# Kernel tuning notes

Hardware: AMD Instinct MI355X
Metric: run time of the kernel (lower is better)

The kernel has to match this reference:

```python
import jax, jax.numpy as jnp
import numpy as np

C = 256
RED = 8
DQK = C // RED  # 32


def setup_inputs() -> dict:
    key = jax.random.key(0)
    ks = jax.random.split(key, 8)
    B, H, W = 8, 64, 64
    x = jax.random.normal(ks[0], (B, C, H, W), dtype=jnp.float32)
    # 1x1 conv weights stored as [out, in]; biases [out]
    Wq = jax.random.normal(ks[1], (DQK, C), dtype=jnp.float32) * 0.02
    bq = jax.random.normal(ks[2], (DQK,), dtype=jnp.float32) * 0.02
    Wk = jax.random.normal(ks[3], (DQK, C), dtype=jnp.float32) * 0.02
    bk = jax.random.normal(ks[4], (DQK,), dtype=jnp.float32) * 0.02
    Wv = jax.random.normal(ks[5], (C, C), dtype=jnp.float32) * 0.02
    bv = jax.random.normal(ks[6], (C,), dtype=jnp.float32) * 0.02
    gamma = jax.random.normal(ks[7], (1,), dtype=jnp.float32) * 0.1
    return {"x": x, "Wq": Wq, "bq": bq, "Wk": Wk, "bk": bk, "Wv": Wv, "bv": bv, "gamma": gamma}


def reference(x, Wq, bq, Wk, bk, Wv, bv, gamma):
    B, Cc, H, W = x.shape
    N = H * W
    xf = x.reshape(B, Cc, N)                       # (B, C, N)
    # 1x1 convs == per-pixel dense projections
    q = jnp.einsum('dc,bcn->bdn', Wq, xf) + bq[None, :, None]   # (B, d, N)
    k = jnp.einsum('dc,bcn->bdn', Wk, xf) + bk[None, :, None]   # (B, d, N)
    v = jnp.einsum('ec,bcn->ben', Wv, xf) + bv[None, :, None]   # (B, C, N)
    # energy[b,i,j] = q[b,:,i] . k[b,:,j]; softmax over j (no scaling, SAGAN-style)
    energy = jnp.einsum('bdi,bdj->bij', q, k)      # (B, N, N)
    attn = jax.nn.softmax(energy, axis=-1)
    # out[b,c,i] = sum_j v[b,c,j] * attn[b,i,j]
    out = jnp.einsum('bcj,bij->bci', v, attn)      # (B, C, N)
    out = out.reshape(B, Cc, H, W)
    return gamma[0] * out + x
```

## Files before the change

kernel.cpp:

```cpp
#include <hip/hip_runtime.h>

#define NB 8
#define CCH 256
#define DQK 32
#define NPIX 4096

typedef __attribute__((ext_vector_type(8))) short short8;
typedef __attribute__((ext_vector_type(4))) float f32x4;

static __device__ __forceinline__ unsigned short f2bf(float f) {
  unsigned int u = __builtin_bit_cast(unsigned int, f);
  u += 0x7FFFu + ((u >> 16) & 1u);
  return (unsigned short)(u >> 16);
}

__global__ __launch_bounds__(256) void proj_kernel(
    const float* __restrict__ x,
    const float* __restrict__ Wq, const float* __restrict__ bq,
    const float* __restrict__ Wk, const float* __restrict__ bk,
    const float* __restrict__ Wv, const float* __restrict__ bv,
    unsigned short* __restrict__ Qb, unsigned short* __restrict__ Kb,
    unsigned short* __restrict__ Vb) {
  __shared__ unsigned short xs[CCH * 65];
  const int t = threadIdx.x;
  const int b = blockIdx.x >> 6;
  const int i0 = (blockIdx.x & 63) * 64;
  const float* xb = x + (size_t)b * CCH * NPIX + i0;
  {
    const int ii = (t & 15) * 4;
    const int cb = t >> 4;
#pragma unroll
    for (int rep = 0; rep < 16; ++rep) {
      const int c = cb + 16 * rep;
      const float4 v = *(const float4*)(xb + (size_t)c * NPIX + ii);
      unsigned short* dst = &xs[c * 65 + ii];
      dst[0] = f2bf(v.x); dst[1] = f2bf(v.y); dst[2] = f2bf(v.z); dst[3] = f2bf(v.w);
    }
  }
  __syncthreads();
  const int w = t >> 6, l = t & 63;
  const int lc = l & 15, lg = l >> 4;
  const int m0w = 80 * w;
  f32x4 acc[5][4];
#pragma unroll
  for (int mt = 0; mt < 5; ++mt)
#pragma unroll
    for (int nt = 0; nt < 4; ++nt) acc[mt][nt] = (f32x4){0.f, 0.f, 0.f, 0.f};

#pragma unroll
  for (int kk = 0; kk < 8; ++kk) {
    const int kbase = kk * 32 + lg * 8;
    short8 af[5];
#pragma unroll
    for (int mt = 0; mt < 5; ++mt) {
      const int m = m0w + mt * 16 + lc;
      const float* wrow;
      if (m < 32) wrow = Wq + (size_t)m * CCH;
      else if (m < 64) wrow = Wk + (size_t)(m - 32) * CCH;
      else wrow = Wv + (size_t)(m - 64) * CCH;
      const float4 w0 = *(const float4*)(wrow + kbase);
      const float4 w1 = *(const float4*)(wrow + kbase + 4);
      short8 a;
      a[0] = (short)f2bf(w0.x); a[1] = (short)f2bf(w0.y);
      a[2] = (short)f2bf(w0.z); a[3] = (short)f2bf(w0.w);
      a[4] = (short)f2bf(w1.x); a[5] = (short)f2bf(w1.y);
      a[6] = (short)f2bf(w1.z); a[7] = (short)f2bf(w1.w);
      af[mt] = a;
    }
#pragma unroll
    for (int nt = 0; nt < 4; ++nt) {
      const int iL = nt * 16 + lc;
      short8 bfv;
#pragma unroll
      for (int j = 0; j < 8; ++j)
        bfv[j] = (short)xs[(kbase + j) * 65 + iL];
#pragma unroll
      for (int mt = 0; mt < 5; ++mt)
        acc[mt][nt] = __builtin_amdgcn_mfma_f32_16x16x32_bf16(af[mt], bfv, acc[mt][nt], 0, 0, 0);
    }
  }
#pragma unroll
  for (int mt = 0; mt < 5; ++mt) {
    const int mbase = m0w + mt * 16;
#pragma unroll
    for (int jj = 0; jj < 4; ++jj) {
      const int m = mbase + lg * 4 + jj;
      float bias;
      if (m < 32) bias = bq[m];
      else if (m < 64) bias = bk[m - 32];
      else bias = bv[m - 64];
#pragma unroll
      for (int nt = 0; nt < 4; ++nt) {
        const int i = i0 + nt * 16 + lc;
        const unsigned short h = f2bf(acc[mt][nt][jj] + bias);
        if (m < 32)      Qb[((size_t)b * NPIX + i) * DQK + m] = h;
        else if (m < 64) Kb[((size_t)b * NPIX + i) * DQK + (m - 32)] = h;
        else             Vb[((size_t)b * CCH + (m - 64)) * NPIX + i] = h;
      }
    }
  }
}

__global__ __launch_bounds__(256) void attn_kernel(
    const unsigned short* __restrict__ Qb,
    const unsigned short* __restrict__ Kb,
    const unsigned short* __restrict__ Vb,
    const float* __restrict__ x,
    const float* __restrict__ gammap,
    float* __restrict__ out) {
  __shared__ unsigned short Plds[64 * 64];
  __shared__ float tsc[4][2][16][17];
  __shared__ float l_lds[64];
  const int t = threadIdx.x;
  const int w = t >> 6, l = t & 63;
  const int lc = l & 15, lg = l >> 4;
  const int b = blockIdx.x >> 6;
  const int q0 = (blockIdx.x & 63) * 64;

  const unsigned short* Qbb = Qb + (size_t)b * NPIX * DQK;
  const unsigned short* Kbb = Kb + (size_t)b * NPIX * DQK;
  const unsigned short* Vbb = Vb + (size_t)b * CCH * NPIX;

  const short8 qa = *(const short8*)(Qbb + (size_t)(q0 + 16 * w + lc) * DQK + lg * 8);

  f32x4 acc[4][4];
#pragma unroll
  for (int mt = 0; mt < 4; ++mt)
#pragma unroll
    for (int ct = 0; ct < 4; ++ct) acc[mt][ct] = (f32x4){0.f, 0.f, 0.f, 0.f};
  float l_acc[4] = {0.f, 0.f, 0.f, 0.f};
  const f32x4 zero4 = {0.f, 0.f, 0.f, 0.f};

  for (int ks = 0; ks < 64; ++ks) {
    const int k0 = ks * 64;
    float p[4][4];
    float psum[4] = {0.f, 0.f, 0.f, 0.f};
#pragma unroll
    for (int kt = 0; kt < 4; ++kt) {
      const short8 kf = *(const short8*)(Kbb + (size_t)(k0 + kt * 16 + lc) * DQK + lg * 8);
      const f32x4 s = __builtin_amdgcn_mfma_f32_16x16x32_bf16(qa, kf, zero4, 0, 0, 0);
#pragma unroll
      for (int jj = 0; jj < 4; ++jj) {
        const float pe = __expf(s[jj]);
        p[kt][jj] = pe;
        psum[jj] += pe;
      }
    }
#pragma unroll
    for (int jj = 0; jj < 4; ++jj) {
      float v = psum[jj];
      v += __shfl_xor(v, 1);
      v += __shfl_xor(v, 2);
      v += __shfl_xor(v, 4);
      v += __shfl_xor(v, 8);
      l_acc[jj] += v;
    }
#pragma unroll
    for (int kt = 0; kt < 4; ++kt) {
      const int kb = kt * 16 + lc;
#pragma unroll
      for (int jj = 0; jj < 4; ++jj) {
        const int qb = 16 * w + lg * 4 + jj;
        Plds[qb * 64 + (kb ^ ((qb & 7) << 3))] = f2bf(p[kt][jj]);
      }
    }
    __syncthreads();
#pragma unroll
    for (int ks2 = 0; ks2 < 2; ++ks2) {
      short8 pa[4];
#pragma unroll
      for (int mt = 0; mt < 4; ++mt) {
        const int qb = 16 * mt + lc;
        const int ke = 32 * ks2 + 8 * lg;
        pa[mt] = *(const short8*)&Plds[qb * 64 + (ke ^ ((qb & 7) << 3))];
      }
#pragma unroll
      for (int ct = 0; ct < 4; ++ct) {
        const int c = 64 * w + 16 * ct + lc;
        const short8 vf = *(const short8*)(Vbb + (size_t)c * NPIX + (k0 + 32 * ks2 + 8 * lg));
#pragma unroll
        for (int mt = 0; mt < 4; ++mt)
          acc[mt][ct] = __builtin_amdgcn_mfma_f32_16x16x32_bf16(pa[mt], vf, acc[mt][ct], 0, 0, 0);
      }
    }
    __syncthreads();
  }

  if (lc == 0) {
#pragma unroll
    for (int jj = 0; jj < 4; ++jj) l_lds[16 * w + lg * 4 + jj] = l_acc[jj];
  }
  __syncthreads();

  const float g = gammap[0];
  float linv[4][4];
#pragma unroll
  for (int mt = 0; mt < 4; ++mt)
#pragma unroll
    for (int jj = 0; jj < 4; ++jj) linv[mt][jj] = 1.0f / l_lds[16 * mt + lg * 4 + jj];

  const float* xbp = x + (size_t)b * CCH * NPIX;
  float* ob = out + (size_t)b * CCH * NPIX;
#pragma unroll
  for (int mt = 0; mt < 4; ++mt) {
#pragma unroll
    for (int ct = 0; ct < 4; ++ct) {
      const int pb = (mt * 4 + ct) & 1;
#pragma unroll
      for (int jj = 0; jj < 4; ++jj)
        tsc[w][pb][lg * 4 + jj][lc] = g * acc[mt][ct][jj] * linv[mt][jj];
#pragma unroll
      for (int r = 0; r < 4; ++r) {
        const int cl = lg + 4 * r;
        const float v = tsc[w][pb][lc][cl];
        const size_t idx = (size_t)(64 * w + 16 * ct + cl) * NPIX + (size_t)(q0 + 16 * mt + lc);
        ob[idx] = v + xbp[idx];
      }
    }
  }
}

extern "C" void kernel_launch(void* const* d_in, const int* in_sizes, int n_in,
                              void* d_out, int out_size, void* d_ws, size_t ws_size,
                              hipStream_t stream) {
  (void)in_sizes; (void)n_in; (void)out_size; (void)ws_size;
  const float* x     = (const float*)d_in[0];
  const float* Wq    = (const float*)d_in[1];
  const float* bq    = (const float*)d_in[2];
  const float* Wk    = (const float*)d_in[3];
  const float* bk    = (const float*)d_in[4];
  const float* Wv    = (const float*)d_in[5];
  const float* bv    = (const float*)d_in[6];
  const float* gamma = (const float*)d_in[7];

  unsigned short* Qb = (unsigned short*)d_ws;
  unsigned short* Kb = Qb + (size_t)NB * NPIX * DQK;
  unsigned short* Vb = Kb + (size_t)NB * NPIX * DQK;

  proj_kernel<<<512, 256, 0, stream>>>(x, Wq, bq, Wk, bk, Wv, bv, Qb, Kb, Vb);
  attn_kernel<<<512, 256, 0, stream>>>(Qb, Kb, Vb, x, gamma, (float*)d_out);
}
```

Measured before the change: 310.2 us.

## Pre-convert weights, swizzle x tile, vectorize stores, software-pipeline attention K/QK

Adds a small kernel that converts the weights to bf16 once, so the projection kernel loads bf16 weight fragments directly instead of reconverting them in every block. The x tile is stored pixel-major with an XOR swizzle so each B fragment is a single 16-byte LDS read, and Q/K outputs are written as 4-wide vectors. In the attention kernel, the QK^T and exp for the next key block are computed after the PV MFMAs and the V fragments are loaded up front, so loads and exp overlap the matrix work. The row-sum shuffle reduction moves to after the loop. This adds an extra launch and more registers.

After: 270.3 us. -12.9%, faster.

```diff
diff --git a/kernel.cpp b/kernel.cpp
--- a/kernel.cpp
+++ b/kernel.cpp
@@ -7,6 +7,7 @@
 
 typedef __attribute__((ext_vector_type(8))) short short8;
 typedef __attribute__((ext_vector_type(4))) float f32x4;
+typedef __attribute__((ext_vector_type(4))) unsigned short ushort4v;
 
 static __device__ __forceinline__ unsigned short f2bf(float f) {
   unsigned int u = __builtin_bit_cast(unsigned int, f);
@@ -14,14 +15,28 @@
   return (unsigned short)(u >> 16);
 }
 
+__global__ __launch_bounds__(256) void wconv_kernel(
+    const float* __restrict__ Wq, const float* __restrict__ Wk,
+    const float* __restrict__ Wv, unsigned short* __restrict__ Wbf) {
+  const int e = (blockIdx.x * 256 + threadIdx.x) * 4;
+  const int m = e >> 8, c = e & 255;
+  const float* src;
+  if (m < 32) src = Wq + (size_t)m * CCH;
+  else if (m < 64) src = Wk + (size_t)(m - 32) * CCH;
+  else src = Wv + (size_t)(m - 64) * CCH;
+  const float4 v = *(const float4*)(src + c);
+  ushort4v o;
+  o[0] = f2bf(v.x); o[1] = f2bf(v.y); o[2] = f2bf(v.z); o[3] = f2bf(v.w);
+  *(ushort4v*)(Wbf + e) = o;
+}
+
 __global__ __launch_bounds__(256) void proj_kernel(
-    const float* __restrict__ x,
-    const float* __restrict__ Wq, const float* __restrict__ bq,
-    const float* __restrict__ Wk, const float* __restrict__ bk,
-    const float* __restrict__ Wv, const float* __restrict__ bv,
+    const float* __restrict__ x, const unsigned short* __restrict__ Wbf,
+    const float* __restrict__ bq, const float* __restrict__ bk,
+    const float* __restrict__ bv,
     unsigned short* __restrict__ Qb, unsigned short* __restrict__ Kb,
     unsigned short* __restrict__ Vb) {
-  __shared__ unsigned short xs[CCH * 65];
+  __shared__ unsigned short xs[64 * 256];
   const int t = threadIdx.x;
   const int b = blockIdx.x >> 6;
   const int i0 = (blockIdx.x & 63) * 64;
@@ -29,12 +44,17 @@
   {
     const int ii = (t & 15) * 4;
     const int cb = t >> 4;
+    const int sw8 = ((ii >> 2) & 7) << 3;
 #pragma unroll
     for (int rep = 0; rep < 16; ++rep) {
       const int c = cb + 16 * rep;
       const float4 v = *(const float4*)(xb + (size_t)c * NPIX + ii);
-      unsigned short* dst = &xs[c * 65 + ii];
-      dst[0] = f2bf(v.x); dst[1] = f2bf(v.y); dst[2] = f2bf(v.z); dst[3] = f2bf(v.w);
+      const float vv[4] = {v.x, v.y, v.z, v.w};
+#pragma unroll
+      for (int d = 0; d < 4; ++d) {
+        const int cc = (c ^ sw8) ^ ((d & 1) << 4);
+        xs[(ii + d) * 256 + cc] = f2bf(vv[d]);
+      }
     }
   }
   __syncthreads();
@@ -49,31 +69,16 @@
 
 #pragma unroll
   for (int kk = 0; kk < 8; ++kk) {
-    const int kbase = kk * 32 + lg * 8;
     short8 af[5];
 #pragma unroll
-    for (int mt = 0; mt < 5; ++mt) {
-      const int m = m0w + mt * 16 + lc;
-      const float* wrow;
-      if (m < 32) wrow = Wq + (size_t)m * CCH;
-      else if (m < 64) wrow = Wk + (size_t)(m - 32) * CCH;
-      else wrow = Wv + (size_t)(m - 64) * CCH;
-      const float4 w0 = *(const float4*)(wrow + kbase);
-      const float4 w1 = *(const float4*)(wrow + kbase + 4);
-      short8 a;
-      a[0] = (short)f2bf(w0.x); a[1] = (short)f2bf(w0.y);
-      a[2] = (short)f2bf(w0.z); a[3] = (short)f2bf(w0.w);
-      a[4] = (short)f2bf(w1.x); a[5] = (short)f2bf(w1.y);
-      a[6] = (short)f2bf(w1.z); a[7] = (short)f2bf(w1.w);
-      af[mt] = a;
-    }
+    for (int mt = 0; mt < 5; ++mt)
+      af[mt] = *(const short8*)(Wbf + (size_t)(m0w + mt * 16 + lc) * CCH + kk * 32 + lg * 8);
 #pragma unroll
     for (int nt = 0; nt < 4; ++nt) {
-      const int iL = nt * 16 + lc;
-      short8 bfv;
-#pragma unroll
-      for (int j = 0; j < 8; ++j)
-        bfv[j] = (short)xs[(kbase + j) * 65 + iL];
+      const int i = nt * 16 + lc;
+      const int s = (4 * nt + (lc >> 2)) & 7;
+      const int cc = ((kk * 32 + lg * 8) ^ (s << 3)) ^ ((lc & 1) << 4);
+      const short8 bfv = *(const short8*)&xs[i * 256 + cc];
 #pragma unroll
       for (int mt = 0; mt < 5; ++mt)
         acc[mt][nt] = __builtin_amdgcn_mfma_f32_16x16x32_bf16(af[mt], bfv, acc[mt][nt], 0, 0, 0);
@@ -82,20 +87,31 @@
 #pragma unroll
   for (int mt = 0; mt < 5; ++mt) {
     const int mbase = m0w + mt * 16;
-#pragma unroll
-    for (int jj = 0; jj < 4; ++jj) {
-      const int m = mbase + lg * 4 + jj;
-      float bias;
-      if (m < 32) bias = bq[m];
-      else if (m < 64) bias = bk[m - 32];
-      else bias = bv[m - 64];
+    const int mrow = mbase + 4 * lg;
+    if (mbase < 64) {
+      const float* bias = (mbase < 32) ? (bq + mrow) : (bk + (mrow - 32));
+      unsigned short* dst = (mbase < 32) ? (Qb + (size_t)b * NPIX * DQK + mrow)
+                                         : (Kb + (size_t)b * NPIX * DQK + (mrow - 32));
+      const float b0 = bias[0], b1 = bias[1], b2 = bias[2], b3 = bias[3];
 #pragma unroll
       for (int nt = 0; nt < 4; ++nt) {
         const int i = i0 + nt * 16 + lc;
-        const unsigned short h = f2bf(acc[mt][nt][jj] + bias);
-        if (m < 32)      Qb[((size_t)b * NPIX + i) * DQK + m] = h;
-        else if (m < 64) Kb[((size_t)b * NPIX + i) * DQK + (m - 32)] = h;
-        else             Vb[((size_t)b * CCH + (m - 64)) * NPIX + i] = h;
+        ushort4v o;
+        o[0] = f2bf(acc[mt][nt][0] + b0);
+        o[1] = f2bf(acc[mt][nt][1] + b1);
+        o[2] = f2bf(acc[mt][nt][2] + b2);
+        o[3] = f2bf(acc[mt][nt][3] + b3);
+        *(ushort4v*)(dst + (size_t)i * DQK) = o;
+      }
+    } else {
+      const int vrow = mbase - 64 + 4 * lg;
+#pragma unroll
+      for (int jj = 0; jj < 4; ++jj) {
+        const float bias = bv[vrow + jj];
+        unsigned short* vdst = Vb + ((size_t)b * CCH + vrow + jj) * NPIX + i0;
+#pragma unroll
+        for (int nt = 0; nt < 4; ++nt)
+          vdst[nt * 16 + lc] = f2bf(acc[mt][nt][jj] + bias);
       }
     }
   }
@@ -118,53 +134,57 @@
   const int q0 = (blockIdx.x & 63) * 64;
 
   const unsigned short* Qbb = Qb + (size_t)b * NPIX * DQK;
-  const unsigned short* Kbb = Kb + (size_t)b * NPIX * DQK;
-  const unsigned short* Vbb = Vb + (size_t)b * CCH * NPIX;
+  const unsigned short* Kl = Kb + (size_t)b * NPIX * DQK + (size_t)lc * DQK + lg * 8;
+  const unsigned short* Vl = Vb + ((size_t)b * CCH + 64 * w + lc) * NPIX + lg * 8;
 
   const short8 qa = *(const short8*)(Qbb + (size_t)(q0 + 16 * w + lc) * DQK + lg * 8);
+  const f32x4 zero4 = {0.f, 0.f, 0.f, 0.f};
 
   f32x4 acc[4][4];
 #pragma unroll
   for (int mt = 0; mt < 4; ++mt)
 #pragma unroll
     for (int ct = 0; ct < 4; ++ct) acc[mt][ct] = (f32x4){0.f, 0.f, 0.f, 0.f};
-  float l_acc[4] = {0.f, 0.f, 0.f, 0.f};
-  const f32x4 zero4 = {0.f, 0.f, 0.f, 0.f};
+  float psum[4] = {0.f, 0.f, 0.f, 0.f};
+  unsigned short pu[4][4];
+
+#pragma unroll
+  for (int kt = 0; kt < 4; ++kt) {
+    const short8 kf = *(const short8*)(Kl + (size_t)(kt * 16) * DQK);
+    const f32x4 s = __builtin_amdgcn_mfma_f32_16x16x32_bf16(qa, kf, zero4, 0, 0, 0);
+#pragma unroll
+    for (int jj = 0; jj < 4; ++jj) {
+      const float pe = __expf(s[jj]);
+      psum[jj] += pe;
+      pu[kt][jj] = f2bf(pe);
+    }
+  }
 
   for (int ks = 0; ks < 64; ++ks) {
     const int k0 = ks * 64;
-    float p[4][4];
-    float psum[4] = {0.f, 0.f, 0.f, 0.f};
-#pragma unroll
-    for (int kt = 0; kt < 4; ++kt) {
-      const short8 kf = *(const short8*)(Kbb + (size_t)(k0 + kt * 16 + lc) * DQK + lg * 8);
-      const f32x4 s = __builtin_amdgcn_mfma_f32_16x16x32_bf16(qa, kf, zero4, 0, 0, 0);
-#pragma unroll
-      for (int jj = 0; jj < 4; ++jj) {
-        const float pe = __expf(s[jj]);
-        p[kt][jj] = pe;
-        psum[jj] += pe;
-      }
-    }
-#pragma unroll
-    for (int jj = 0; jj < 4; ++jj) {
-      float v = psum[jj];
-      v += __shfl_xor(v, 1);
-      v += __shfl_xor(v, 2);
-      v += __shfl_xor(v, 4);
-      v += __shfl_xor(v, 8);
-      l_acc[jj] += v;
-    }
 #pragma unroll
     for (int kt = 0; kt < 4; ++kt) {
       const int kb = kt * 16 + lc;
 #pragma unroll
       for (int jj = 0; jj < 4; ++jj) {
         const int qb = 16 * w + lg * 4 + jj;
-        Plds[qb * 64 + (kb ^ ((qb & 7) << 3))] = f2bf(p[kt][jj]);
+        Plds[qb * 64 + (kb ^ ((qb & 7) << 3))] = pu[kt][jj];
       }
     }
     __syncthreads();
+    const bool notlast = (ks < 63);
+    short8 kfn[4];
+    if (notlast) {
+#pragma unroll
+      for (int kt = 0; kt < 4; ++kt)
+        kfn[kt] = *(const short8*)(Kl + (size_t)(k0 + 64 + kt * 16) * DQK);
+    }
+    short8 vf[2][4];
+#pragma unroll
+    for (int ks2 = 0; ks2 < 2; ++ks2)
+#pragma unroll
+      for (int ct = 0; ct < 4; ++ct)
+        vf[ks2][ct] = *(const short8*)(Vl + (size_t)(16 * ct) * NPIX + k0 + 32 * ks2);
 #pragma unroll
     for (int ks2 = 0; ks2 < 2; ++ks2) {
       short8 pa[4];
@@ -175,20 +195,34 @@
         pa[mt] = *(const short8*)&Plds[qb * 64 + (ke ^ ((qb & 7) << 3))];
       }
 #pragma unroll
-      for (int ct = 0; ct < 4; ++ct) {
-        const int c = 64 * w + 16 * ct + lc;
-        const short8 vf = *(const short8*)(Vbb + (size_t)c * NPIX + (k0 + 32 * ks2 + 8 * lg));
+      for (int ct = 0; ct < 4; ++ct)
 #pragma unroll
         for (int mt = 0; mt < 4; ++mt)
-          acc[mt][ct] = __builtin_amdgcn_mfma_f32_16x16x32_bf16(pa[mt], vf, acc[mt][ct], 0, 0, 0);
+          acc[mt][ct] = __builtin_amdgcn_mfma_f32_16x16x32_bf16(pa[mt], vf[ks2][ct], acc[mt][ct], 0, 0, 0);
+    }
+    if (notlast) {
+#pragma unroll
+      for (int kt = 0; kt < 4; ++kt) {
+        const f32x4 s = __builtin_amdgcn_mfma_f32_16x16x32_bf16(qa, kfn[kt], zero4, 0, 0, 0);
+#pragma unroll
+        for (int jj = 0; jj < 4; ++jj) {
+          const float pe = __expf(s[jj]);
+          psum[jj] += pe;
+          pu[kt][jj] = f2bf(pe);
+        }
       }
     }
     __syncthreads();
   }
 
-  if (lc == 0) {
-#pragma unroll
-    for (int jj = 0; jj < 4; ++jj) l_lds[16 * w + lg * 4 + jj] = l_acc[jj];
+#pragma unroll
+  for (int jj = 0; jj < 4; ++jj) {
+    float v = psum[jj];
+    v += __shfl_xor(v, 1);
+    v += __shfl_xor(v, 2);
+    v += __shfl_xor(v, 4);
+    v += __shfl_xor(v, 8);
+    if (lc == 0) l_lds[16 * w + lg * 4 + jj] = v;
   }
   __syncthreads();
 
@@ -233,10 +267,12 @@
   const float* bv    = (const float*)d_in[6];
   const float* gamma = (const float*)d_in[7];
 
-  unsigned short* Qb = (unsigned short*)d_ws;
-  unsigned short* Kb = Qb + (size_t)NB * NPIX * DQK;
-  unsigned short* Vb = Kb + (size_t)NB * NPIX * DQK;
-
-  proj_kernel<<<512, 256, 0, stream>>>(x, Wq, bq, Wk, bk, Wv, bv, Qb, Kb, Vb);
+  unsigned short* Wbf = (unsigned short*)d_ws;
+  unsigned short* Qb  = Wbf + 320 * CCH;
+  unsigned short* Kb  = Qb + (size_t)NB * NPIX * DQK;
+  unsigned short* Vb  = Kb + (size_t)NB * NPIX * DQK;
+
+  wconv_kernel<<<80, 256, 0, stream>>>(Wq, Wk, Wv, Wbf);
+  proj_kernel<<<512, 256, 0, stream>>>(x, Wbf, bq, bk, bv, Qb, Kb, Vb);
   attn_kernel<<<512, 256, 0, stream>>>(Qb, Kb, Vb, x, gamma, (float*)d_out);
 }
```
